# Performance work log

Hardware: AMD Instinct MI355X
Metric: run time of the kernel (lower is better)

The kernel has to match this reference:

```python
import jax, jax.numpy as jnp
import numpy as np

H = 64      # h_dim
E = 64      # embedding_dim
L = 100     # latent_dim
T = 30      # seq_len
DT = 0.03

def _leaky(x):
    return jnp.where(x >= 0, x, 0.01 * x)  # nn.LeakyReLU default slope

def _mlp(h, Ws, bs, Wf, bf):
    # 3 stacked [H,H] LeakyReLU layers + final [L,H] layer, LeakyReLU after EVERY layer (as in source)
    for i in range(Ws.shape[0]):
        h = _leaky(h @ Ws[i].T + bs[i])
    return _leaky(h @ Wf.T + bf)

def _lstm_step(h, c, gates):
    # torch LSTM gate order: i, f, g, o
    i, f, g, o = jnp.split(gates, 4, axis=-1)
    c = jax.nn.sigmoid(f) * c + jax.nn.sigmoid(i) * jnp.tanh(g)
    h = jax.nn.sigmoid(o) * jnp.tanh(c)
    return h, c

def _forward(expert_traj, init_state, eps,
             W_se, b_se,
             W_ih_e, W_hh_e, b_ih_e, b_hh_e,
             mean_Ws, mean_bs, mean_Wf, mean_bf,
             lv_Ws, lv_bs, lv_Wf, lv_bf,
             W_init, b_init,
             W_ih_d, W_hh_d, b_ih_d, b_hh_d,
             W_c, b_c):
    B = expert_traj.shape[0]
    # --- encode: relative positions ---
    rel_xy = jnp.concatenate([expert_traj[:, :1, :2],
                              expert_traj[:, 1:, :2] - expert_traj[:, :-1, :2]], axis=1)
    inp = jnp.concatenate([rel_xy, expert_traj[:, :, 2:]], axis=-1)  # [B,T,4]
    emb = inp @ W_se.T + b_se                                        # [B,T,E]
    x_seq = jnp.swapaxes(emb, 0, 1)                                  # [T,B,E] seq-major
    # precompute input projection for all timesteps in one GEMM
    xp = x_seq @ W_ih_e.T + (b_ih_e + b_hh_e)                        # [T,B,4H]
    h0 = jnp.zeros((B, H), dtype=expert_traj.dtype)
    c0 = jnp.zeros((B, H), dtype=expert_traj.dtype)
    def enc_step(carry, xp_t):
        h, c = carry
        h, c = _lstm_step(h, c, xp_t + h @ W_hh_e.T)
        return (h, c), None
    (hT, _), _ = jax.lax.scan(enc_step, (h0, c0), xp)
    mu = _mlp(hT, mean_Ws, mean_bs, mean_Wf, mean_bf)                # [B,L]
    log_var = _mlp(hT, lv_Ws, lv_bs, lv_Wf, lv_bf)                   # [B,L]
    # --- reparameterize + tanh ---
    z = jnp.tanh(eps * jnp.exp(0.5 * log_var) + mu)
    # --- decode ---
    dh = z @ W_init.T + b_init                                       # [B,H], h0 = c0 = dh
    bias_d = b_ih_d + b_hh_d
    def dec_step(carry, _):
        h, c, prev = carry
        xe = prev @ W_se.T + b_se                                    # spatial embedding of state
        h, c = _lstm_step(h, c, xe @ W_ih_d.T + h @ W_hh_d.T + bias_d)
        ctrl = h @ W_c.T + b_c                                       # [B,2]
        pedal = ctrl[:, 0]
        steer = jnp.clip(ctrl[:, 1], -0.5, 0.5)
        x_t, y_t, psi, v = prev[:, 0], prev[:, 1], prev[:, 2], prev[:, 3]
        v1 = jnp.clip(v + pedal * DT, 0.0, 30.0)
        psi_dot = jnp.clip(v * jnp.tan(steer) / 2.5, -3.14 / 2, 3.14 / 2)
        cur = jnp.stack([x_t + v * jnp.cos(psi) * DT,
                         y_t + v * jnp.sin(psi) * DT,
                         psi + psi_dot * DT,
                         v1], axis=1)
        return (h, c, cur), cur
    _, traj = jax.lax.scan(dec_step, (dh, dh, init_state), None, length=T)
    recons = jnp.swapaxes(traj, 0, 1)                                # [B,T,4]
    return recons, expert_traj, mu, log_var

def setup_inputs() -> dict:
    key = jax.random.key(0)
    ks = jax.random.split(key, 32)
    B = 16384
    s = 0.05
    def p(k, shape):
        return jax.random.normal(k, shape, dtype=jnp.float32) * s
    return {
        "expert_traj": jax.random.normal(ks[0], (B, T, 4), dtype=jnp.float32),
        "init_state": jax.random.normal(ks[1], (B, 4), dtype=jnp.float32),
        "eps": jax.random.normal(ks[2], (B, L), dtype=jnp.float32),
        "W_se": p(ks[3], (E, 4)), "b_se": p(ks[4], (E,)),
        "W_ih_e": p(ks[5], (4 * H, E)), "W_hh_e": p(ks[6], (4 * H, H)),
        "b_ih_e": p(ks[7], (4 * H,)), "b_hh_e": p(ks[8], (4 * H,)),
        "mean_Ws": p(ks[9], (3, H, H)), "mean_bs": p(ks[10], (3, H)),
        "mean_Wf": p(ks[11], (L, H)), "mean_bf": p(ks[12], (L,)),
        "lv_Ws": p(ks[13], (3, H, H)), "lv_bs": p(ks[14], (3, H)),
        "lv_Wf": p(ks[15], (L, H)), "lv_bf": p(ks[16], (L,)),
        "W_init": p(ks[17], (H, L)), "b_init": p(ks[18], (H,)),
        "W_ih_d": p(ks[19], (4 * H, E)), "W_hh_d": p(ks[20], (4 * H, H)),
        "b_ih_d": p(ks[21], (4 * H,)), "b_hh_d": p(ks[22], (4 * H,)),
        "W_c": p(ks[23], (2, H)), "b_c": p(ks[24], (2,)),
    }

def reference(expert_traj, init_state, eps,
              W_se, b_se,
              W_ih_e, W_hh_e, b_ih_e, b_hh_e,
              mean_Ws, mean_bs, mean_Wf, mean_bf,
              lv_Ws, lv_bs, lv_Wf, lv_bf,
              W_init, b_init,
              W_ih_d, W_hh_d, b_ih_d, b_hh_d,
              W_c, b_c):
    return _forward(expert_traj, init_state, eps,
                    W_se, b_se,
                    W_ih_e, W_hh_e, b_ih_e, b_hh_e,
                    mean_Ws, mean_bs, mean_Wf, mean_bf,
                    lv_Ws, lv_bs, lv_Wf, lv_bf,
                    W_init, b_init,
                    W_ih_d, W_hh_d, b_ih_d, b_hh_d,
                    W_c, b_c)
```

## Files before the change

### kernel.cpp

```cpp
#include <hip/hip_runtime.h>

typedef unsigned short u16;
typedef unsigned int u32;
typedef __attribute__((ext_vector_type(8))) short bf16x8;
typedef __attribute__((ext_vector_type(4))) float f32x4;

#define B_TOT 16384
#define RR 16
#define NBLK (B_TOT / RR)
#define TT 30
#define LL 100
#define DTC 0.03f
#define L2E 1.44269504088896f

#define HST 104
#define HBUF_U16 (RR * HST)

#define OFF_H   0
#define OFF_XB  6656
#define OFF_Z   11264
#define OFF_U   15616
#define SMEM_SZ 19456

#define WS_WHHE  0
#define WS_WHHD  18432
#define WS_MWS   36864
#define WS_LWS   49152
#define WS_MWF   61440
#define WS_LWF   67840
#define WS_WINIT 74240
#define WS_TOTAL 82432

__device__ __forceinline__ float bf2f(u16 u) {
    union { u32 i; float f; } v; v.i = ((u32)u) << 16; return v.f;
}
__device__ __forceinline__ u16 f2bf(float f) {
    union { float f; u32 i; } v; v.f = f;
    return (u16)((v.i + 0x7FFFu + ((v.i >> 16) & 1u)) >> 16);
}
__device__ __forceinline__ float rcpf(float x) { return __builtin_amdgcn_rcpf(x); }
__device__ __forceinline__ float ex2(float x) { return __builtin_amdgcn_exp2f(x); }
__device__ __forceinline__ float tanh_(float x) {
    x = fminf(fmaxf(x, -15.f), 15.f);
    float e = __expf(2.f * x);
    return (e - 1.f) * rcpf(e + 1.f);
}
__device__ __forceinline__ float leaky(float x) { return x >= 0.f ? x : 0.01f * x; }
__device__ __forceinline__ f32x4 mfma16(bf16x8 a, bf16x8 b, f32x4 c) {
    return __builtin_amdgcn_mfma_f32_16x16x32_bf16(a, b, c, 0, 0, 0);
}

__global__ void setup_kernel(
    const float* __restrict__ W_se, const float* __restrict__ b_se,
    const float* __restrict__ W_ih_e, const float* __restrict__ W_hh_e,
    const float* __restrict__ b_ih_e, const float* __restrict__ b_hh_e,
    const float* __restrict__ W_ih_d, const float* __restrict__ W_hh_d,
    const float* __restrict__ b_ih_d, const float* __restrict__ b_hh_d,
    const float* __restrict__ mean_Ws, const float* __restrict__ lv_Ws,
    const float* __restrict__ mean_Wf, const float* __restrict__ lv_Wf,
    const float* __restrict__ W_init, u16* __restrict__ ws)
{
    const int gid = blockIdx.x * 256 + threadIdx.x;
    const int nth = gridDim.x * 256;
    for (int i = gid; i < 512; i += nth) {
        int which = i >> 8, row = i & 255, g = row >> 6;
        float s = (g == 2) ? 2.f * L2E : L2E;
        const float* wih = (which ? W_ih_d : W_ih_e) + row * 64;
        float f0=0,f1=0,f2=0,f3=0,fb=0;
        for (int e = 0; e < 64; ++e) {
            float w = wih[e];
            f0 = fmaf(w, W_se[e*4+0], f0);
            f1 = fmaf(w, W_se[e*4+1], f1);
            f2 = fmaf(w, W_se[e*4+2], f2);
            f3 = fmaf(w, W_se[e*4+3], f3);
            fb = fmaf(w, b_se[e], fb);
        }
        fb += (which ? b_ih_d : b_ih_e)[row] + (which ? b_hh_d : b_hh_e)[row];
        u16* dst = ws + (which ? WS_WHHD : WS_WHHE) + row * 72 + 64;
        dst[0]=f2bf(f0*s); dst[1]=f2bf(f1*s); dst[2]=f2bf(f2*s); dst[3]=f2bf(f3*s);
        dst[4]=f2bf(fb*s); dst[5]=0; dst[6]=0; dst[7]=0;
    }
    for (int i = gid; i < 2*16384; i += nth) {
        int which = i >= 16384;
        int j = which ? i - 16384 : i;
        int row = j >> 6, k = j & 63, g = row >> 6;
        float s = (g == 2) ? 2.f * L2E : L2E;
        const float* whh = which ? W_hh_d : W_hh_e;
        ws[(which ? WS_WHHD : WS_WHHE) + row*72 + k] = f2bf(whh[j] * s);
    }
    for (int i = gid; i < 12288; i += nth) {
        ws[WS_MWS + i] = f2bf(mean_Ws[i]);
        ws[WS_LWS + i] = f2bf(lv_Ws[i]);
    }
    for (int i = gid; i < 6400; i += nth) {
        ws[WS_MWF + i] = f2bf(mean_Wf[i]);
        ws[WS_LWF + i] = f2bf(lv_Wf[i]);
    }
    for (int i = gid; i < 8192; i += nth) {
        int r = i >> 7, k = i & 127;
        ws[WS_WINIT + i] = (k < LL) ? f2bf(W_init[r*LL + k]) : (u16)0;
    }
}

__global__ __launch_bounds__(256, 6) void vae_lstm_kernel(
    const float* __restrict__ expert, const float* __restrict__ init_state,
    const float* __restrict__ eps, const u16* __restrict__ ws,
    const float* __restrict__ mean_bs, const float* __restrict__ mean_bf,
    const float* __restrict__ lv_bs, const float* __restrict__ lv_bf,
    const float* __restrict__ b_init, const float* __restrict__ W_c,
    const float* __restrict__ b_c,
    float* __restrict__ out_recons, float* __restrict__ out_expert,
    float* __restrict__ out_mu, float* __restrict__ out_lv)
{
    const int tid = threadIdx.x;
    const int b0g = blockIdx.x * RR;
    const int wv = tid >> 6;
    const int lane = tid & 63;
    const int lcol = lane & 15;
    const int quad = lane >> 4;
    const int jcol = wv * 16 + lcol;

    __shared__ __align__(16) char smem[SMEM_SZ];
    u16* Hbuf  = (u16*)(smem + OFF_H);
    u16* XB0   = (u16*)(smem + OFF_XB);
    u16* XB1   = XB0 + RR * 72;
    u16* zBuf  = (u16*)(smem + OFF_Z);
    u16* inp   = (u16*)(smem + OFF_U);
    u16* muB   = (u16*)(smem + OFF_U);
    float* sRaw  = (float*)(smem + OFF_XB);
    float* sPrev = (float*)(smem + OFF_XB);
    float* sWc   = (float*)(smem + OFF_XB + 256);

    {
        const int base = b0g * (TT*4);
        u32* hz = (u32*)Hbuf;
        for (int idx = tid; idx < HBUF_U16; idx += 256) hz[idx] = 0;
        for (int idx = tid; idx < RR*TT*4; idx += 256) {
            float v = expert[base + idx];
            sRaw[idx] = v;
            out_expert[base + idx] = v;
        }
        __syncthreads();
        for (int idx = tid; idx < RR*TT*4; idx += 256) {
            int q = idx % (TT*4);
            int k = q & 3, t = q >> 2;
            int row = idx / (TT*4);
            float v = sRaw[idx];
            if (k < 2 && t > 0) v -= sRaw[idx - 4];
            u16 hv = f2bf(v);
            inp[idx] = hv;
            if (t == 0) Hbuf[row*HST + 64 + k] = hv;
            if (q == 0) {
                Hbuf[row*HST + 68] = 0x3F80;
                Hbuf[HBUF_U16 + row*HST + 68] = 0x3F80;
            }
        }
        __syncthreads();
    }

    float creg[4] = {0.f, 0.f, 0.f, 0.f};
    bf16x8 bw[4][3];

    auto build_bw = [&](const u16* wsW) {
#pragma unroll
        for (int g = 0; g < 4; ++g) {
            const u16* wr = wsW + (g*64 + jcol) * 72;
            bw[g][0] = *(const bf16x8*)(wr + quad*8);
            bw[g][1] = *(const bf16x8*)(wr + 32 + quad*8);
            if (quad == 0) {
                bw[g][2] = *(const bf16x8*)(wr + 64);
            } else {
                bf16x8 z;
#pragma unroll
                for (int j = 0; j < 8; ++j) z[j] = 0;
                bw[g][2] = z;
            }
        }
    };

    auto lstm_step = [&](const u16* Hc, u16* Hn) {
        bf16x8 a0 = *(const bf16x8*)(Hc + lcol*HST + quad*8);
        bf16x8 a1 = *(const bf16x8*)(Hc + lcol*HST + 32 + quad*8);
        bf16x8 a2 = *(const bf16x8*)(Hc + lcol*HST + 64 + quad*8);
        f32x4 acc[4];
#pragma unroll
        for (int g = 0; g < 4; ++g) {
            f32x4 z = {0.f, 0.f, 0.f, 0.f};
            z = mfma16(a0, bw[g][0], z);
            z = mfma16(a1, bw[g][1], z);
            acc[g] = mfma16(a2, bw[g][2], z);
        }
#pragma unroll
        for (int r = 0; r < 4; ++r) {
            float Ei = ex2(-acc[0][r]);
            float Ef = ex2(-acc[1][r]);
            float Eg = ex2(-acc[2][r]);
            float Eo = ex2(-acc[3][r]);
            float P = (1.f + Ei) * (1.f + Eg);
            float Q = 1.f + Ef;
            float num = fmaf(creg[r], P, (1.f - Eg) * Q);
            float c = num * rcpf(P * Q);
            creg[r] = c;
            float Ec = ex2(-2.f * L2E * c);
            float h = (1.f - Ec) * rcpf((1.f + Eo) * (1.f + Ec));
            Hn[(quad*4 + r)*HST + jcol] = f2bf(h);
        }
    };

    build_bw(ws + WS_WHHE);
    for (int stp = 0; stp < TT; ++stp) {
        const u16* Hc = Hbuf + (stp & 1) * HBUF_U16;
        u16* Hn = Hbuf + ((stp + 1) & 1) * HBUF_U16;
        lstm_step(Hc, Hn);
        if (tid < 64 && stp < TT-1) {
            int row = tid >> 2, k = tid & 3;
            Hn[row*HST + 64 + k] = inp[row*(TT*4) + (stp+1)*4 + k];
        }
        __syncthreads();
    }

    {
        u32* zb = (u32*)zBuf;
        for (int idx = tid; idx < RR*136/2; idx += 256) zb[idx] = 0;
    }

    auto mlp_hidden = [&](const u16* inB, int inStride, u16* outB,
                          const u16* wsW, const float* bg) {
        float bv = bg[jcol];
        const u16* wr = wsW + jcol*64;
        bf16x8 bb0 = *(const bf16x8*)(wr + quad*8);
        bf16x8 bb1 = *(const bf16x8*)(wr + 32 + quad*8);
        f32x4 acc = {bv, bv, bv, bv};
        bf16x8 a0 = *(const bf16x8*)(inB + lcol*inStride + quad*8);
        bf16x8 a1 = *(const bf16x8*)(inB + lcol*inStride + 32 + quad*8);
        acc = mfma16(a0, bb0, acc);
        acc = mfma16(a1, bb1, acc);
#pragma unroll
        for (int r = 0; r < 4; ++r)
            outB[(quad*4 + r)*72 + jcol] = f2bf(leaky(acc[r]));
        __syncthreads();
    };

    auto mlp_final = [&](const u16* inB, const u16* wsW, const float* bg, int mode) {
#pragma unroll
        for (int ni = 0; ni < 2; ++ni) {
            int nt = wv + ni*4;
            if (nt >= 7) continue;
            int n = nt*16 + lcol;
            bool ok = (n < LL);
            float bv = ok ? bg[n] : 0.f;
            bf16x8 bb0, bb1;
            if (ok) {
                const u16* wr = wsW + n*64;
                bb0 = *(const bf16x8*)(wr + quad*8);
                bb1 = *(const bf16x8*)(wr + 32 + quad*8);
            } else {
#pragma unroll
                for (int j = 0; j < 8; ++j) { bb0[j] = 0; bb1[j] = 0; }
            }
            f32x4 acc = {bv, bv, bv, bv};
            bf16x8 a0 = *(const bf16x8*)(inB + lcol*72 + quad*8);
            bf16x8 a1 = *(const bf16x8*)(inB + lcol*72 + 32 + quad*8);
            acc = mfma16(a0, bb0, acc);
            acc = mfma16(a1, bb1, acc);
            if (ok) {
#pragma unroll
                for (int r = 0; r < 4; ++r) {
                    int m = quad*4 + r;
                    float vv = leaky(acc[r]);
                    size_t gi = (size_t)(b0g + m) * LL + n;
                    if (mode == 0) {
                        muB[m*LL + n] = f2bf(vv);
                        out_mu[gi] = vv;
                    } else {
                        out_lv[gi] = vv;
                        float mu = bf2f(muB[m*LL + n]);
                        float zv = tanh_(fmaf(eps[gi], __expf(0.5f * vv), mu));
                        zBuf[m*136 + n] = f2bf(zv);
                    }
                }
            }
        }
        __syncthreads();
    };

    mlp_hidden(Hbuf, HST, XB0, ws + WS_MWS, mean_bs);
    mlp_hidden(XB0, 72, XB1, ws + WS_MWS + 4096, mean_bs + 64);
    mlp_hidden(XB1, 72, XB0, ws + WS_MWS + 8192, mean_bs + 128);
    mlp_final(XB0, ws + WS_MWF, mean_bf, 0);
    mlp_hidden(Hbuf, HST, XB0, ws + WS_LWS, lv_bs);
    mlp_hidden(XB0, 72, XB1, ws + WS_LWS + 4096, lv_bs + 64);
    mlp_hidden(XB1, 72, XB0, ws + WS_LWS + 8192, lv_bs + 128);
    mlp_final(XB0, ws + WS_LWF, lv_bf, 1);

    {
        float bv = b_init[jcol];
        const u16* wr = ws + WS_WINIT + jcol*128;
        f32x4 acc = {bv, bv, bv, bv};
#pragma unroll
        for (int kt = 0; kt < 4; ++kt) {
            bf16x8 az = *(const bf16x8*)(zBuf + lcol*136 + kt*32 + quad*8);
            bf16x8 bi = *(const bf16x8*)(wr + kt*32 + quad*8);
            acc = mfma16(az, bi, acc);
        }
#pragma unroll
        for (int r = 0; r < 4; ++r) {
            creg[r] = acc[r];
            Hbuf[(quad*4 + r)*HST + jcol] = f2bf(acc[r]);
        }
        __syncthreads();
        if (tid < RR*4) {
            float v = init_state[b0g*4 + tid];
            sPrev[tid] = v;
            Hbuf[(tid >> 2)*HST + 64 + (tid & 3)] = f2bf(v);
        }
        if (tid < 128) sWc[tid] = W_c[tid];
        __syncthreads();
    }

    build_bw(ws + WS_WHHD);
    const float bc0 = b_c[0], bc1 = b_c[1];

    for (int stp = 0; stp < TT; ++stp) {
        const u16* Hc = Hbuf + (stp & 1) * HBUF_U16;
        u16* Hn = Hbuf + ((stp + 1) & 1) * HBUF_U16;
        lstm_step(Hc, Hn);
        __syncthreads();
        if (tid < 64) {
            int row = tid >> 2, kq = tid & 3;
            const u16* hr = Hn + row*HST + kq*16;
            bf16x8 h0 = *(const bf16x8*)(hr);
            bf16x8 h1 = *(const bf16x8*)(hr + 8);
            const float4* w0 = (const float4*)(sWc + kq*16);
            const float4* w1 = (const float4*)(sWc + 64 + kq*16);
            float a0 = 0.f, a1 = 0.f;
#pragma unroll
            for (int p = 0; p < 2; ++p) {
                float4 wa = w0[2*p], wb = w0[2*p+1];
                float4 va = w1[2*p], vb = w1[2*p+1];
                bf16x8 hh = p ? h1 : h0;
                float hf[8];
#pragma unroll
                for (int j = 0; j < 8; ++j) hf[j] = bf2f((u16)hh[j]);
                a0 = fmaf(hf[0], wa.x, a0); a0 = fmaf(hf[1], wa.y, a0);
                a0 = fmaf(hf[2], wa.z, a0); a0 = fmaf(hf[3], wa.w, a0);
                a0 = fmaf(hf[4], wb.x, a0); a0 = fmaf(hf[5], wb.y, a0);
                a0 = fmaf(hf[6], wb.z, a0); a0 = fmaf(hf[7], wb.w, a0);
                a1 = fmaf(hf[0], va.x, a1); a1 = fmaf(hf[1], va.y, a1);
                a1 = fmaf(hf[2], va.z, a1); a1 = fmaf(hf[3], va.w, a1);
                a1 = fmaf(hf[4], vb.x, a1); a1 = fmaf(hf[5], vb.y, a1);
                a1 = fmaf(hf[6], vb.z, a1); a1 = fmaf(hf[7], vb.w, a1);
            }
            a0 += __shfl_xor(a0, 1); a1 += __shfl_xor(a1, 1);
            a0 += __shfl_xor(a0, 2); a1 += __shfl_xor(a1, 2);
            if (kq == 0) {
                float pedal = a0 + bc0;
                float steer = fminf(fmaxf(a1 + bc1, -0.5f), 0.5f);
                float4 pv = *(const float4*)(sPrev + row*4);
                float x = pv.x, y = pv.y, psi = pv.z, v = pv.w;
                float v1 = fminf(fmaxf(v + pedal * DTC, 0.f), 30.f);
                float sn, cs;
                __sincosf(psi, &sn, &cs);
                float psid = fminf(fmaxf(v * __tanf(steer) * 0.4f, -1.57f), 1.57f);
                float nx = fmaf(v * cs, DTC, x);
                float ny = fmaf(v * sn, DTC, y);
                float npsi = fmaf(psid, DTC, psi);
                float4 o; o.x = nx; o.y = ny; o.z = npsi; o.w = v1;
                *(float4*)(sPrev + row*4) = o;
                *(float4*)(out_recons + ((size_t)(b0g + row) * TT + stp) * 4) = o;
                u32 lo = (u32)f2bf(nx) | ((u32)f2bf(ny) << 16);
                u32 hi = (u32)f2bf(npsi) | ((u32)f2bf(v1) << 16);
                uint2 pk; pk.x = lo; pk.y = hi;
                *(uint2*)(Hn + row*HST + 64) = pk;
            }
        }
        __syncthreads();
    }
}

extern "C" void kernel_launch(void* const* d_in, const int* in_sizes, int n_in,
                              void* d_out, int out_size, void* d_ws, size_t ws_size,
                              hipStream_t stream) {
    (void)in_sizes; (void)n_in; (void)ws_size; (void)out_size;
    const float* expert    = (const float*)d_in[0];
    const float* init_st   = (const float*)d_in[1];
    const float* eps       = (const float*)d_in[2];
    const float* W_se      = (const float*)d_in[3];
    const float* b_se      = (const float*)d_in[4];
    const float* W_ih_e    = (const float*)d_in[5];
    const float* W_hh_e    = (const float*)d_in[6];
    const float* b_ih_e    = (const float*)d_in[7];
    const float* b_hh_e    = (const float*)d_in[8];
    const float* mean_Ws   = (const float*)d_in[9];
    const float* mean_bs   = (const float*)d_in[10];
    const float* mean_Wf   = (const float*)d_in[11];
    const float* mean_bf   = (const float*)d_in[12];
    const float* lv_Ws     = (const float*)d_in[13];
    const float* lv_bs     = (const float*)d_in[14];
    const float* lv_Wf     = (const float*)d_in[15];
    const float* lv_bf     = (const float*)d_in[16];
    const float* W_init    = (const float*)d_in[17];
    const float* b_init    = (const float*)d_in[18];
    const float* W_ih_d    = (const float*)d_in[19];
    const float* W_hh_d    = (const float*)d_in[20];
    const float* b_ih_d    = (const float*)d_in[21];
    const float* b_hh_d    = (const float*)d_in[22];
    const float* W_c       = (const float*)d_in[23];
    const float* b_c       = (const float*)d_in[24];

    float* out = (float*)d_out;
    const size_t n_traj = (size_t)B_TOT * TT * 4;
    const size_t n_lat  = (size_t)B_TOT * LL;
    float* out_recons = out;
    float* out_expert = out + n_traj;
    float* out_mu     = out + 2 * n_traj;
    float* out_lv     = out + 2 * n_traj + n_lat;

    u16* ws = (u16*)d_ws;

    setup_kernel<<<64, 256, 0, stream>>>(
        W_se, b_se, W_ih_e, W_hh_e, b_ih_e, b_hh_e,
        W_ih_d, W_hh_d, b_ih_d, b_hh_d,
        mean_Ws, lv_Ws, mean_Wf, lv_Wf, W_init, ws);

    vae_lstm_kernel<<<NBLK, 256, 0, stream>>>(
        expert, init_st, eps, ws,
        mean_bs, mean_bf, lv_bs, lv_bf, b_init, W_c, b_c,
        out_recons, out_expert, out_mu, out_lv);
}
```

Before: 260.7 us.

## Process 32 rows per block to reuse LSTM weight registers across two M-tiles

Doubles the batch rows per block from 16 to 32, so each wave runs two 16-row MFMA tiles against the same register-resident recurrent weights. This halves the block count and amortizes the weight loads and per-step barriers over more rows. Shared memory is resized, the occupancy hint drops from 6 to 2, and the helper loops gain an outer M-tile loop. Float-to-bf16 conversion also changes from round-to-nearest to truncation, which is cheaper but slightly less accurate.

```diff
diff --git a/kernel.cpp b/kernel.cpp
--- a/kernel.cpp
+++ b/kernel.cpp
@@ -6,7 +6,7 @@
 typedef __attribute__((ext_vector_type(4))) float f32x4;
 
 #define B_TOT 16384
-#define RR 16
+#define RR 32
 #define NBLK (B_TOT / RR)
 #define TT 30
 #define LL 100
@@ -17,10 +17,10 @@
 #define HBUF_U16 (RR * HST)
 
 #define OFF_H   0
-#define OFF_XB  6656
-#define OFF_Z   11264
-#define OFF_U   15616
-#define SMEM_SZ 19456
+#define OFF_XB  13312
+#define OFF_Z   22528
+#define OFF_U   31232
+#define SMEM_SZ 38912
 
 #define WS_WHHE  0
 #define WS_WHHD  18432
@@ -37,6 +37,10 @@
 __device__ __forceinline__ u16 f2bf(float f) {
     union { float f; u32 i; } v; v.f = f;
     return (u16)((v.i + 0x7FFFu + ((v.i >> 16) & 1u)) >> 16);
+}
+__device__ __forceinline__ u16 f2bf_t(float f) {
+    union { float f; u32 i; } v; v.f = f;
+    return (u16)(v.i >> 16);
 }
 __device__ __forceinline__ float rcpf(float x) { return __builtin_amdgcn_rcpf(x); }
 __device__ __forceinline__ float ex2(float x) { return __builtin_amdgcn_exp2f(x); }
@@ -102,7 +106,7 @@
     }
 }
 
-__global__ __launch_bounds__(256, 6) void vae_lstm_kernel(
+__global__ __launch_bounds__(256, 2) void vae_lstm_kernel(
     const float* __restrict__ expert, const float* __restrict__ init_state,
     const float* __restrict__ eps, const u16* __restrict__ ws,
     const float* __restrict__ mean_bs, const float* __restrict__ mean_bf,
@@ -129,7 +133,7 @@
     u16* muB   = (u16*)(smem + OFF_U);
     float* sRaw  = (float*)(smem + OFF_XB);
     float* sPrev = (float*)(smem + OFF_XB);
-    float* sWc   = (float*)(smem + OFF_XB + 256);
+    float* sWc   = (float*)(smem + OFF_XB + 512);
 
     {
         const int base = b0g * (TT*4);
@@ -158,7 +162,9 @@
         __syncthreads();
     }
 
-    float creg[4] = {0.f, 0.f, 0.f, 0.f};
+    float creg[8];
+#pragma unroll
+    for (int u = 0; u < 8; ++u) creg[u] = 0.f;
     bf16x8 bw[4][3];
 
     auto build_bw = [&](const u16* wsW) {
@@ -179,32 +185,37 @@
     };
 
     auto lstm_step = [&](const u16* Hc, u16* Hn) {
-        bf16x8 a0 = *(const bf16x8*)(Hc + lcol*HST + quad*8);
-        bf16x8 a1 = *(const bf16x8*)(Hc + lcol*HST + 32 + quad*8);
-        bf16x8 a2 = *(const bf16x8*)(Hc + lcol*HST + 64 + quad*8);
-        f32x4 acc[4];
-#pragma unroll
-        for (int g = 0; g < 4; ++g) {
-            f32x4 z = {0.f, 0.f, 0.f, 0.f};
-            z = mfma16(a0, bw[g][0], z);
-            z = mfma16(a1, bw[g][1], z);
-            acc[g] = mfma16(a2, bw[g][2], z);
-        }
-#pragma unroll
-        for (int r = 0; r < 4; ++r) {
-            float Ei = ex2(-acc[0][r]);
-            float Ef = ex2(-acc[1][r]);
-            float Eg = ex2(-acc[2][r]);
-            float Eo = ex2(-acc[3][r]);
-            float P = (1.f + Ei) * (1.f + Eg);
-            float Q = 1.f + Ef;
-            float num = fmaf(creg[r], P, (1.f - Eg) * Q);
-            float c = num * rcpf(P * Q);
-            creg[r] = c;
-            float Ec = ex2(-2.f * L2E * c);
-            float h = (1.f - Ec) * rcpf((1.f + Eo) * (1.f + Ec));
-            Hn[(quad*4 + r)*HST + jcol] = f2bf(h);
-        }
+        f32x4 acc[2][4];
+#pragma unroll
+        for (int c = 0; c < 2; ++c) {
+            bf16x8 a0 = *(const bf16x8*)(Hc + (c*16 + lcol)*HST + quad*8);
+            bf16x8 a1 = *(const bf16x8*)(Hc + (c*16 + lcol)*HST + 32 + quad*8);
+            bf16x8 a2 = *(const bf16x8*)(Hc + (c*16 + lcol)*HST + 64 + quad*8);
+#pragma unroll
+            for (int g = 0; g < 4; ++g) {
+                f32x4 z = {0.f, 0.f, 0.f, 0.f};
+                z = mfma16(a0, bw[g][0], z);
+                z = mfma16(a1, bw[g][1], z);
+                acc[c][g] = mfma16(a2, bw[g][2], z);
+            }
+        }
+#pragma unroll
+        for (int c = 0; c < 2; ++c)
+#pragma unroll
+            for (int r = 0; r < 4; ++r) {
+                float Ei = ex2(-acc[c][0][r]);
+                float Ef = ex2(-acc[c][1][r]);
+                float Eg = ex2(-acc[c][2][r]);
+                float Eo = ex2(-acc[c][3][r]);
+                float P = (1.f + Ei) * (1.f + Eg);
+                float Q = 1.f + Ef;
+                float num = fmaf(creg[c*4 + r], P, (1.f - Eg) * Q);
+                float cc = num * rcpf(P * Q);
+                creg[c*4 + r] = cc;
+                float Ec = ex2(-2.f * L2E * cc);
+                float h = (1.f - Ec) * rcpf((1.f + Eo) * (1.f + Ec));
+                Hn[(c*16 + quad*4 + r)*HST + jcol] = f2bf_t(h);
+            }
     };
 
     build_bw(ws + WS_WHHE);
@@ -212,7 +223,7 @@
         const u16* Hc = Hbuf + (stp & 1) * HBUF_U16;
         u16* Hn = Hbuf + ((stp + 1) & 1) * HBUF_U16;
         lstm_step(Hc, Hn);
-        if (tid < 64 && stp < TT-1) {
+        if (tid < 128 && stp < TT-1) {
             int row = tid >> 2, k = tid & 3;
             Hn[row*HST + 64 + k] = inp[row*(TT*4) + (stp+1)*4 + k];
         }
@@ -230,14 +241,17 @@
         const u16* wr = wsW + jcol*64;
         bf16x8 bb0 = *(const bf16x8*)(wr + quad*8);
         bf16x8 bb1 = *(const bf16x8*)(wr + 32 + quad*8);
-        f32x4 acc = {bv, bv, bv, bv};
-        bf16x8 a0 = *(const bf16x8*)(inB + lcol*inStride + quad*8);
-        bf16x8 a1 = *(const bf16x8*)(inB + lcol*inStride + 32 + quad*8);
-        acc = mfma16(a0, bb0, acc);
-        acc = mfma16(a1, bb1, acc);
-#pragma unroll
-        for (int r = 0; r < 4; ++r)
-            outB[(quad*4 + r)*72 + jcol] = f2bf(leaky(acc[r]));
+#pragma unroll
+        for (int Mt = 0; Mt < 2; ++Mt) {
+            f32x4 acc = {bv, bv, bv, bv};
+            bf16x8 a0 = *(const bf16x8*)(inB + (Mt*16 + lcol)*inStride + quad*8);
+            bf16x8 a1 = *(const bf16x8*)(inB + (Mt*16 + lcol)*inStride + 32 + quad*8);
+            acc = mfma16(a0, bb0, acc);
+            acc = mfma16(a1, bb1, acc);
+#pragma unroll
+            for (int r = 0; r < 4; ++r)
+                outB[(Mt*16 + quad*4 + r)*72 + jcol] = f2bf_t(leaky(acc[r]));
+        }
         __syncthreads();
     };
 
@@ -258,25 +272,28 @@
 #pragma unroll
                 for (int j = 0; j < 8; ++j) { bb0[j] = 0; bb1[j] = 0; }
             }
-            f32x4 acc = {bv, bv, bv, bv};
-            bf16x8 a0 = *(const bf16x8*)(inB + lcol*72 + quad*8);
-            bf16x8 a1 = *(const bf16x8*)(inB + lcol*72 + 32 + quad*8);
-            acc = mfma16(a0, bb0, acc);
-            acc = mfma16(a1, bb1, acc);
-            if (ok) {
-#pragma unroll
-                for (int r = 0; r < 4; ++r) {
-                    int m = quad*4 + r;
-                    float vv = leaky(acc[r]);
-                    size_t gi = (size_t)(b0g + m) * LL + n;
-                    if (mode == 0) {
-                        muB[m*LL + n] = f2bf(vv);
-                        out_mu[gi] = vv;
-                    } else {
-                        out_lv[gi] = vv;
-                        float mu = bf2f(muB[m*LL + n]);
-                        float zv = tanh_(fmaf(eps[gi], __expf(0.5f * vv), mu));
-                        zBuf[m*136 + n] = f2bf(zv);
+#pragma unroll
+            for (int Mt = 0; Mt < 2; ++Mt) {
+                f32x4 acc = {bv, bv, bv, bv};
+                bf16x8 a0 = *(const bf16x8*)(inB + (Mt*16 + lcol)*72 + quad*8);
+                bf16x8 a1 = *(const bf16x8*)(inB + (Mt*16 + lcol)*72 + 32 + quad*8);
+                acc = mfma16(a0, bb0, acc);
+                acc = mfma16(a1, bb1, acc);
+                if (ok) {
+#pragma unroll
+                    for (int r = 0; r < 4; ++r) {
+                        int m = Mt*16 + quad*4 + r;
+                        float vv = leaky(acc[r]);
+                        size_t gi = (size_t)(b0g + m) * LL + n;
+                        if (mode == 0) {
+                            muB[m*LL + n] = f2bf_t(vv);
+                            out_mu[gi] = vv;
+                        } else {
+                            out_lv[gi] = vv;
+                            float mu = bf2f(muB[m*LL + n]);
+                            float zv = tanh_(fmaf(eps[gi], __expf(0.5f * vv), mu));
+                            zBuf[m*136 + n] = f2bf_t(zv);
+                        }
                     }
                 }
             }
@@ -296,17 +313,20 @@
     {
         float bv = b_init[jcol];
         const u16* wr = ws + WS_WINIT + jcol*128;
-        f32x4 acc = {bv, bv, bv, bv};
-#pragma unroll
-        for (int kt = 0; kt < 4; ++kt) {
-            bf16x8 az = *(const bf16x8*)(zBuf + lcol*136 + kt*32 + quad*8);
-            bf16x8 bi = *(const bf16x8*)(wr + kt*32 + quad*8);
-            acc = mfma16(az, bi, acc);
-        }
-#pragma unroll
-        for (int r = 0; r < 4; ++r) {
-            creg[r] = acc[r];
-            Hbuf[(quad*4 + r)*HST + jcol] = f2bf(acc[r]);
+#pragma unroll
+        for (int Mt = 0; Mt < 2; ++Mt) {
+            f32x4 acc = {bv, bv, bv, bv};
+#pragma unroll
+            for (int kt = 0; kt < 4; ++kt) {
+                bf16x8 az = *(const bf16x8*)(zBuf + (Mt*16 + lcol)*136 + kt*32 + quad*8);
+                bf16x8 bi = *(const bf16x8*)(wr + kt*32 + quad*8);
+                acc = mfma16(az, bi, acc);
+            }
+#pragma unroll
+            for (int r = 0; r < 4; ++r) {
+                creg[Mt*4 + r] = acc[r];
+                Hbuf[(Mt*16 + quad*4 + r)*HST + jcol] = f2bf_t(acc[r]);
+            }
         }
         __syncthreads();
         if (tid < RR*4) {
@@ -326,7 +346,7 @@
         u16* Hn = Hbuf + ((stp + 1) & 1) * HBUF_U16;
         lstm_step(Hc, Hn);
         __syncthreads();
-        if (tid < 64) {
+        if (tid < 128) {
             int row = tid >> 2, kq = tid & 3;
             const u16* hr = Hn + row*HST + kq*16;
             bf16x8 h0 = *(const bf16x8*)(hr);
```

Measured after the change: 219.2 us. -15.9%, faster.

## Run each 16-row tile on a single wavefront with MFMA control head

Applied to the files above, without the earlier changes.

Shrinks each block from four wavefronts to one, so a single wave holds all 64 hidden columns' recurrent weights in registers and loops over four column groups. The aim is to make barriers nearly free and remove cross-wave sync in the 60 serial LSTM steps. The decoder control projection moves from scalar FMAs plus shuffles to two MFMAs. Several bf16 conversions switch from round-to-nearest to truncation. In exchange there are far more registers per wave (192 weight vectors), less parallelism per sequential step, and slightly lower precision from truncation.

```diff
diff --git a/kernel.cpp b/kernel.cpp
--- a/kernel.cpp
+++ b/kernel.cpp
@@ -7,6 +7,7 @@
 
 #define B_TOT 16384
 #define RR 16
+#define BLK 64
 #define NBLK (B_TOT / RR)
 #define TT 30
 #define LL 100
@@ -38,6 +39,10 @@
     union { float f; u32 i; } v; v.f = f;
     return (u16)((v.i + 0x7FFFu + ((v.i >> 16) & 1u)) >> 16);
 }
+__device__ __forceinline__ u16 f2bf_t(float f) {
+    union { float f; u32 i; } v; v.f = f;
+    return (u16)(v.i >> 16);
+}
 __device__ __forceinline__ float rcpf(float x) { return __builtin_amdgcn_rcpf(x); }
 __device__ __forceinline__ float ex2(float x) { return __builtin_amdgcn_exp2f(x); }
 __device__ __forceinline__ float tanh_(float x) {
@@ -48,6 +53,12 @@
 __device__ __forceinline__ float leaky(float x) { return x >= 0.f ? x : 0.01f * x; }
 __device__ __forceinline__ f32x4 mfma16(bf16x8 a, bf16x8 b, f32x4 c) {
     return __builtin_amdgcn_mfma_f32_16x16x32_bf16(a, b, c, 0, 0, 0);
+}
+__device__ __forceinline__ bf16x8 packw(const float* p) {
+    bf16x8 r;
+#pragma unroll
+    for (int j = 0; j < 8; ++j) r[j] = (short)f2bf(p[j]);
+    return r;
 }
 
 __global__ void setup_kernel(
@@ -102,7 +113,7 @@
     }
 }
 
-__global__ __launch_bounds__(256, 6) void vae_lstm_kernel(
+__global__ __launch_bounds__(BLK, 1) void vae_lstm_kernel(
     const float* __restrict__ expert, const float* __restrict__ init_state,
     const float* __restrict__ eps, const u16* __restrict__ ws,
     const float* __restrict__ mean_bs, const float* __restrict__ mean_bf,
@@ -112,13 +123,10 @@
     float* __restrict__ out_recons, float* __restrict__ out_expert,
     float* __restrict__ out_mu, float* __restrict__ out_lv)
 {
-    const int tid = threadIdx.x;
+    const int lane = threadIdx.x;
     const int b0g = blockIdx.x * RR;
-    const int wv = tid >> 6;
-    const int lane = tid & 63;
     const int lcol = lane & 15;
     const int quad = lane >> 4;
-    const int jcol = wv * 16 + lcol;
 
     __shared__ __align__(16) char smem[SMEM_SZ];
     u16* Hbuf  = (u16*)(smem + OFF_H);
@@ -129,19 +137,19 @@
     u16* muB   = (u16*)(smem + OFF_U);
     float* sRaw  = (float*)(smem + OFF_XB);
     float* sPrev = (float*)(smem + OFF_XB);
-    float* sWc   = (float*)(smem + OFF_XB + 256);
+    float* sCtrl = (float*)(smem + OFF_XB + 256);
 
     {
         const int base = b0g * (TT*4);
         u32* hz = (u32*)Hbuf;
-        for (int idx = tid; idx < HBUF_U16; idx += 256) hz[idx] = 0;
-        for (int idx = tid; idx < RR*TT*4; idx += 256) {
+        for (int idx = lane; idx < 2*HBUF_U16/2; idx += BLK) hz[idx] = 0;
+        for (int idx = lane; idx < RR*TT*4; idx += BLK) {
             float v = expert[base + idx];
             sRaw[idx] = v;
             out_expert[base + idx] = v;
         }
         __syncthreads();
-        for (int idx = tid; idx < RR*TT*4; idx += 256) {
+        for (int idx = lane; idx < RR*TT*4; idx += BLK) {
             int q = idx % (TT*4);
             int k = q & 3, t = q >> 2;
             int row = idx / (TT*4);
@@ -158,52 +166,60 @@
         __syncthreads();
     }
 
-    float creg[4] = {0.f, 0.f, 0.f, 0.f};
-    bf16x8 bw[4][3];
+    float creg[16];
+#pragma unroll
+    for (int u = 0; u < 16; ++u) creg[u] = 0.f;
+    bf16x8 bw[4][4][3];
 
     auto build_bw = [&](const u16* wsW) {
 #pragma unroll
-        for (int g = 0; g < 4; ++g) {
-            const u16* wr = wsW + (g*64 + jcol) * 72;
-            bw[g][0] = *(const bf16x8*)(wr + quad*8);
-            bw[g][1] = *(const bf16x8*)(wr + 32 + quad*8);
-            if (quad == 0) {
-                bw[g][2] = *(const bf16x8*)(wr + 64);
-            } else {
-                bf16x8 z;
-#pragma unroll
-                for (int j = 0; j < 8; ++j) z[j] = 0;
-                bw[g][2] = z;
-            }
-        }
+        for (int cg = 0; cg < 4; ++cg)
+#pragma unroll
+            for (int g = 0; g < 4; ++g) {
+                const u16* wr = wsW + (g*64 + cg*16 + lcol) * 72;
+                bw[cg][g][0] = *(const bf16x8*)(wr + quad*8);
+                bw[cg][g][1] = *(const bf16x8*)(wr + 32 + quad*8);
+                if (quad == 0) {
+                    bw[cg][g][2] = *(const bf16x8*)(wr + 64);
+                } else {
+                    bf16x8 z;
+#pragma unroll
+                    for (int j = 0; j < 8; ++j) z[j] = 0;
+                    bw[cg][g][2] = z;
+                }
+            }
     };
 
     auto lstm_step = [&](const u16* Hc, u16* Hn) {
-        bf16x8 a0 = *(const bf16x8*)(Hc + lcol*HST + quad*8);
-        bf16x8 a1 = *(const bf16x8*)(Hc + lcol*HST + 32 + quad*8);
-        bf16x8 a2 = *(const bf16x8*)(Hc + lcol*HST + 64 + quad*8);
-        f32x4 acc[4];
-#pragma unroll
-        for (int g = 0; g < 4; ++g) {
-            f32x4 z = {0.f, 0.f, 0.f, 0.f};
-            z = mfma16(a0, bw[g][0], z);
-            z = mfma16(a1, bw[g][1], z);
-            acc[g] = mfma16(a2, bw[g][2], z);
-        }
-#pragma unroll
-        for (int r = 0; r < 4; ++r) {
-            float Ei = ex2(-acc[0][r]);
-            float Ef = ex2(-acc[1][r]);
-            float Eg = ex2(-acc[2][r]);
-            float Eo = ex2(-acc[3][r]);
-            float P = (1.f + Ei) * (1.f + Eg);
-            float Q = 1.f + Ef;
-            float num = fmaf(creg[r], P, (1.f - Eg) * Q);
-            float c = num * rcpf(P * Q);
-            creg[r] = c;
-            float Ec = ex2(-2.f * L2E * c);
-            float h = (1.f - Ec) * rcpf((1.f + Eo) * (1.f + Ec));
-            Hn[(quad*4 + r)*HST + jcol] = f2bf(h);
+        const u16* hrow = Hc + lcol*HST;
+        bf16x8 a0 = *(const bf16x8*)(hrow + quad*8);
+        bf16x8 a1 = *(const bf16x8*)(hrow + 32 + quad*8);
+        bf16x8 a2 = *(const bf16x8*)(hrow + 64 + quad*8);
+#pragma unroll
+        for (int cg = 0; cg < 4; ++cg) {
+            f32x4 acc[4];
+#pragma unroll
+            for (int g = 0; g < 4; ++g) {
+                f32x4 z = {0.f, 0.f, 0.f, 0.f};
+                z = mfma16(a0, bw[cg][g][0], z);
+                z = mfma16(a1, bw[cg][g][1], z);
+                acc[g] = mfma16(a2, bw[cg][g][2], z);
+            }
+#pragma unroll
+            for (int r = 0; r < 4; ++r) {
+                float Ei = ex2(-acc[0][r]);
+                float Ef = ex2(-acc[1][r]);
+                float Eg = ex2(-acc[2][r]);
+                float Eo = ex2(-acc[3][r]);
+                float P = (1.f + Ei) * (1.f + Eg);
+                float Q = 1.f + Ef;
+                float num = fmaf(creg[cg*4 + r], P, (1.f - Eg) * Q);
+                float cc = num * rcpf(P * Q);
+                creg[cg*4 + r] = cc;
+                float Ec = ex2(-2.f * L2E * cc);
+                float h = (1.f - Ec) * rcpf((1.f + Eo) * (1.f + Ec));
+                Hn[(quad*4 + r)*HST + cg*16 + lcol] = f2bf_t(h);
+            }
         }
     };
 
@@ -212,8 +228,8 @@
         const u16* Hc = Hbuf + (stp & 1) * HBUF_U16;
         u16* Hn = Hbuf + ((stp + 1) & 1) * HBUF_U16;
         lstm_step(Hc, Hn);
-        if (tid < 64 && stp < TT-1) {
-            int row = tid >> 2, k = tid & 3;
+        if (stp < TT-1) {
+            int row = lane >> 2, k = lane & 3;
             Hn[row*HST + 64 + k] = inp[row*(TT*4) + (stp+1)*4 + k];
         }
         __syncthreads();
@@ -221,46 +237,43 @@
 
     {
         u32* zb = (u32*)zBuf;
-        for (int idx = tid; idx < RR*136/2; idx += 256) zb[idx] = 0;
+        for (int idx = lane; idx < RR*136/2; idx += BLK) zb[idx] = 0;
     }
 
     auto mlp_hidden = [&](const u16* inB, int inStride, u16* outB,
                           const u16* wsW, const float* bg) {
-        float bv = bg[jcol];
-        const u16* wr = wsW + jcol*64;
-        bf16x8 bb0 = *(const bf16x8*)(wr + quad*8);
-        bf16x8 bb1 = *(const bf16x8*)(wr + 32 + quad*8);
-        f32x4 acc = {bv, bv, bv, bv};
         bf16x8 a0 = *(const bf16x8*)(inB + lcol*inStride + quad*8);
         bf16x8 a1 = *(const bf16x8*)(inB + lcol*inStride + 32 + quad*8);
-        acc = mfma16(a0, bb0, acc);
-        acc = mfma16(a1, bb1, acc);
-#pragma unroll
-        for (int r = 0; r < 4; ++r)
-            outB[(quad*4 + r)*72 + jcol] = f2bf(leaky(acc[r]));
+#pragma unroll
+        for (int cg = 0; cg < 4; ++cg) {
+            int j = cg*16 + lcol;
+            float bv = bg[j];
+            const u16* wr = wsW + j*64;
+            bf16x8 bb0 = *(const bf16x8*)(wr + quad*8);
+            bf16x8 bb1 = *(const bf16x8*)(wr + 32 + quad*8);
+            f32x4 acc = {bv, bv, bv, bv};
+            acc = mfma16(a0, bb0, acc);
+            acc = mfma16(a1, bb1, acc);
+#pragma unroll
+            for (int r = 0; r < 4; ++r)
+                outB[(quad*4 + r)*72 + j] = f2bf_t(leaky(acc[r]));
+        }
         __syncthreads();
     };
 
     auto mlp_final = [&](const u16* inB, const u16* wsW, const float* bg, int mode) {
-#pragma unroll
-        for (int ni = 0; ni < 2; ++ni) {
-            int nt = wv + ni*4;
-            if (nt >= 7) continue;
+        bf16x8 a0 = *(const bf16x8*)(inB + lcol*72 + quad*8);
+        bf16x8 a1 = *(const bf16x8*)(inB + lcol*72 + 32 + quad*8);
+#pragma unroll
+        for (int nt = 0; nt < 7; ++nt) {
             int n = nt*16 + lcol;
             bool ok = (n < LL);
+            int nc = ok ? n : 0;
             float bv = ok ? bg[n] : 0.f;
-            bf16x8 bb0, bb1;
-            if (ok) {
-                const u16* wr = wsW + n*64;
-                bb0 = *(const bf16x8*)(wr + quad*8);
-                bb1 = *(const bf16x8*)(wr + 32 + quad*8);
-            } else {
-#pragma unroll
-                for (int j = 0; j < 8; ++j) { bb0[j] = 0; bb1[j] = 0; }
-            }
+            const u16* wr = wsW + nc*64;
+            bf16x8 bb0 = *(const bf16x8*)(wr + quad*8);
+            bf16x8 bb1 = *(const bf16x8*)(wr + 32 + quad*8);
             f32x4 acc = {bv, bv, bv, bv};
-            bf16x8 a0 = *(const bf16x8*)(inB + lcol*72 + quad*8);
-            bf16x8 a1 = *(const bf16x8*)(inB + lcol*72 + 32 + quad*8);
             acc = mfma16(a0, bb0, acc);
             acc = mfma16(a1, bb1, acc);
             if (ok) {
@@ -270,13 +283,13 @@
                     float vv = leaky(acc[r]);
                     size_t gi = (size_t)(b0g + m) * LL + n;
                     if (mode == 0) {
-                        muB[m*LL + n] = f2bf(vv);
+                        muB[m*LL + n] = f2bf_t(vv);
                         out_mu[gi] = vv;
                     } else {
                         out_lv[gi] = vv;
                         float mu = bf2f(muB[m*LL + n]);
                         float zv = tanh_(fmaf(eps[gi], __expf(0.5f * vv), mu));
-                        zBuf[m*136 + n] = f2bf(zv);
+                        zBuf[m*136 + n] = f2bf_t(zv);
                     }
                 }
             }
@@ -294,31 +307,49 @@
     mlp_final(XB0, ws + WS_LWF, lv_bf, 1);
 
     {
-        float bv = b_init[jcol];
-        const u16* wr = ws + WS_WINIT + jcol*128;
-        f32x4 acc = {bv, bv, bv, bv};
-#pragma unroll
-        for (int kt = 0; kt < 4; ++kt) {
-            bf16x8 az = *(const bf16x8*)(zBuf + lcol*136 + kt*32 + quad*8);
-            bf16x8 bi = *(const bf16x8*)(wr + kt*32 + quad*8);
-            acc = mfma16(az, bi, acc);
-        }
-#pragma unroll
-        for (int r = 0; r < 4; ++r) {
-            creg[r] = acc[r];
-            Hbuf[(quad*4 + r)*HST + jcol] = f2bf(acc[r]);
-        }
-        __syncthreads();
-        if (tid < RR*4) {
-            float v = init_state[b0g*4 + tid];
-            sPrev[tid] = v;
-            Hbuf[(tid >> 2)*HST + 64 + (tid & 3)] = f2bf(v);
-        }
-        if (tid < 128) sWc[tid] = W_c[tid];
+        bf16x8 az[4];
+#pragma unroll
+        for (int kt = 0; kt < 4; ++kt)
+            az[kt] = *(const bf16x8*)(zBuf + lcol*136 + kt*32 + quad*8);
+#pragma unroll
+        for (int cg = 0; cg < 4; ++cg) {
+            int j = cg*16 + lcol;
+            float bv = b_init[j];
+            const u16* wr = ws + WS_WINIT + j*128;
+            f32x4 acc = {bv, bv, bv, bv};
+#pragma unroll
+            for (int kt = 0; kt < 4; ++kt) {
+                bf16x8 bi = *(const bf16x8*)(wr + kt*32 + quad*8);
+                acc = mfma16(az[kt], bi, acc);
+            }
+#pragma unroll
+            for (int r = 0; r < 4; ++r) {
+                creg[cg*4 + r] = acc[r];
+                Hbuf[(quad*4 + r)*HST + cg*16 + lcol] = f2bf_t(acc[r]);
+            }
+        }
+        __syncthreads();
+        {
+            int row = lane >> 2, k = lane & 3;
+            float v = init_state[b0g*4 + lane];
+            sPrev[lane] = v;
+            Hbuf[row*HST + 64 + k] = f2bf(v);
+        }
         __syncthreads();
     }
 
     build_bw(ws + WS_WHHD);
+    bf16x8 wcb0, wcb1;
+    {
+        bf16x8 z;
+#pragma unroll
+        for (int j = 0; j < 8; ++j) z[j] = 0;
+        wcb0 = z; wcb1 = z;
+        if (lcol < 2) {
+            wcb0 = packw(W_c + lcol*64 + quad*8);
+            wcb1 = packw(W_c + lcol*64 + 32 + quad*8);
+        }
+    }
     const float bc0 = b_c[0], bc1 = b_c[1];
 
     for (int stp = 0; stp < TT; ++stp) {
@@ -326,53 +357,40 @@
         u16* Hn = Hbuf + ((stp + 1) & 1) * HBUF_U16;
         lstm_step(Hc, Hn);
         __syncthreads();
-        if (tid < 64) {
-            int row = tid >> 2, kq = tid & 3;
-            const u16* hr = Hn + row*HST + kq*16;
-            bf16x8 h0 = *(const bf16x8*)(hr);
-            bf16x8 h1 = *(const bf16x8*)(hr + 8);
-            const float4* w0 = (const float4*)(sWc + kq*16);
-            const float4* w1 = (const float4*)(sWc + 64 + kq*16);
-            float a0 = 0.f, a1 = 0.f;
-#pragma unroll
-            for (int p = 0; p < 2; ++p) {
-                float4 wa = w0[2*p], wb = w0[2*p+1];
-                float4 va = w1[2*p], vb = w1[2*p+1];
-                bf16x8 hh = p ? h1 : h0;
-                float hf[8];
-#pragma unroll
-                for (int j = 0; j < 8; ++j) hf[j] = bf2f((u16)hh[j]);
-                a0 = fmaf(hf[0], wa.x, a0); a0 = fmaf(hf[1], wa.y, a0);
-                a0 = fmaf(hf[2], wa.z, a0); a0 = fmaf(hf[3], wa.w, a0);
-                a0 = fmaf(hf[4], wb.x, a0); a0 = fmaf(hf[5], wb.y, a0);
-                a0 = fmaf(hf[6], wb.z, a0); a0 = fmaf(hf[7], wb.w, a0);
-                a1 = fmaf(hf[0], va.x, a1); a1 = fmaf(hf[1], va.y, a1);
-                a1 = fmaf(hf[2], va.z, a1); a1 = fmaf(hf[3], va.w, a1);
-                a1 = fmaf(hf[4], vb.x, a1); a1 = fmaf(hf[5], vb.y, a1);
-                a1 = fmaf(hf[6], vb.z, a1); a1 = fmaf(hf[7], vb.w, a1);
-            }
-            a0 += __shfl_xor(a0, 1); a1 += __shfl_xor(a1, 1);
-            a0 += __shfl_xor(a0, 2); a1 += __shfl_xor(a1, 2);
-            if (kq == 0) {
-                float pedal = a0 + bc0;
-                float steer = fminf(fmaxf(a1 + bc1, -0.5f), 0.5f);
-                float4 pv = *(const float4*)(sPrev + row*4);
-                float x = pv.x, y = pv.y, psi = pv.z, v = pv.w;
-                float v1 = fminf(fmaxf(v + pedal * DTC, 0.f), 30.f);
-                float sn, cs;
-                __sincosf(psi, &sn, &cs);
-                float psid = fminf(fmaxf(v * __tanf(steer) * 0.4f, -1.57f), 1.57f);
-                float nx = fmaf(v * cs, DTC, x);
-                float ny = fmaf(v * sn, DTC, y);
-                float npsi = fmaf(psid, DTC, psi);
-                float4 o; o.x = nx; o.y = ny; o.z = npsi; o.w = v1;
-                *(float4*)(sPrev + row*4) = o;
-                *(float4*)(out_recons + ((size_t)(b0g + row) * TT + stp) * 4) = o;
-                u32 lo = (u32)f2bf(nx) | ((u32)f2bf(ny) << 16);
-                u32 hi = (u32)f2bf(npsi) | ((u32)f2bf(v1) << 16);
-                uint2 pk; pk.x = lo; pk.y = hi;
-                *(uint2*)(Hn + row*HST + 64) = pk;
-            }
+        {
+            const u16* hrow = Hn + lcol*HST;
+            bf16x8 c0 = *(const bf16x8*)(hrow + quad*8);
+            bf16x8 c1 = *(const bf16x8*)(hrow + 32 + quad*8);
+            f32x4 cacc = {0.f, 0.f, 0.f, 0.f};
+            cacc = mfma16(c0, wcb0, cacc);
+            cacc = mfma16(c1, wcb1, cacc);
+            if (lcol < 2) {
+#pragma unroll
+                for (int r = 0; r < 4; ++r)
+                    sCtrl[(quad*4 + r)*2 + lcol] = cacc[r];
+            }
+        }
+        __syncthreads();
+        if (lane < RR) {
+            int row = lane;
+            float pedal = sCtrl[row*2] + bc0;
+            float steer = fminf(fmaxf(sCtrl[row*2 + 1] + bc1, -0.5f), 0.5f);
+            float4 pv = *(const float4*)(sPrev + row*4);
+            float x = pv.x, y = pv.y, psi = pv.z, v = pv.w;
+            float v1 = fminf(fmaxf(v + pedal * DTC, 0.f), 30.f);
+            float sn, cs;
+            __sincosf(psi, &sn, &cs);
+            float psid = fminf(fmaxf(v * __tanf(steer) * 0.4f, -1.57f), 1.57f);
+            float nx = fmaf(v * cs, DTC, x);
+            float ny = fmaf(v * sn, DTC, y);
+            float npsi = fmaf(psid, DTC, psi);
+            float4 o; o.x = nx; o.y = ny; o.z = npsi; o.w = v1;
+            *(float4*)(sPrev + row*4) = o;
+            *(float4*)(out_recons + ((size_t)(b0g + row) * TT + stp) * 4) = o;
+            u32 lo = (u32)f2bf(nx) | ((u32)f2bf(ny) << 16);
+            u32 hi = (u32)f2bf(npsi) | ((u32)f2bf(v1) << 16);
+            uint2 pk; pk.x = lo; pk.y = hi;
+            *(uint2*)(Hn + row*HST + 64) = pk;
         }
         __syncthreads();
     }
@@ -423,7 +441,7 @@
         W_ih_d, W_hh_d, b_ih_d, b_hh_d,
         mean_Ws, lv_Ws, mean_Wf, lv_Wf, W_init, ws);
 
-    vae_lstm_kernel<<<NBLK, 256, 0, stream>>>(
+    vae_lstm_kernel<<<NBLK, BLK, 0, stream>>>(
         expert, init_st, eps, ws,
         mean_bs, mean_bf, lv_bs, lv_bf, b_init, W_c, b_c,
         out_recons, out_expert, out_mu, out_lv);
```

Result: faster. 229.9 us (-11.8%).
